# Optimization experiments

Hardware: AMD Instinct MI355X
Metric: run time of the kernel (lower is better)

The kernel has to match this reference:

```python
import jax, jax.numpy as jnp
from jax import lax
import numpy as np

B, T, Z, H, W = 4, 256, 16, 64, 64

def setup_inputs() -> dict:
    key = jax.random.key(0)
    k1, k2, k3, k4, k5 = jax.random.split(key, 5)
    # per-pixel scalar RNN parameters (nn.RNN(1, 1) per pixel)
    return {
        "x": jax.random.normal(k1, (B, T, Z, H, W), dtype=jnp.float32),
        "w_ih": jax.random.normal(k2, (Z, H, W), dtype=jnp.float32),
        "w_hh": jax.random.normal(k3, (Z, H, W), dtype=jnp.float32),
        "b_ih": jax.random.normal(k4, (Z, H, W), dtype=jnp.float32),
        "b_hh": jax.random.normal(k5, (Z, H, W), dtype=jnp.float32),
    }

def reference(x, w_ih, w_hh, b_ih, b_hh):
    # x: (B, T, Z, H, W). Per-pixel scalar tanh-RNN, h0 = 0:
    #   h_t = tanh(w_ih * x_t + b_ih + w_hh * h_{t-1} + b_hh)
    xt = jnp.moveaxis(x, 1, 0)  # (T, B, Z, H, W) for scan over time
    bias = b_ih + b_hh          # fuse biases once

    def step(h, x_t):
        h_new = jnp.tanh(x_t * w_ih + h * w_hh + bias)
        return h_new, h_new

    h0 = jnp.zeros(xt.shape[1:], dtype=x.dtype)  # (B, Z, H, W)
    _, ys = lax.scan(step, h0, xt)               # ys: (T, B, Z, H, W)
    return jnp.moveaxis(ys, 0, 1)                # (B, T, Z, H, W)
```

## Files before the change

### kernel.cpp

```cpp
#include <hip/hip_runtime.h>


#define RNN_B 4
#define RNN_T 256
#define RNN_ZHW 65536
#define RNN_PG (RNN_ZHW / 4)

__global__ __launch_bounds__(256) void pixel_rnn_kernel(
    const float* __restrict__ x,
    const float* __restrict__ w_ih,
    const float* __restrict__ w_hh,
    const float* __restrict__ b_ih,
    const float* __restrict__ b_hh,
    float* __restrict__ out)
{
    const int g  = blockIdx.x * 256 + threadIdx.x;
    const int b  = g >> 14;
    const int pg = g & (RNN_PG - 1);
    const int p  = pg << 2;

    const float4 wi = *(const float4*)(w_ih + p);
    const float4 wh = *(const float4*)(w_hh + p);
    const float4 bi = *(const float4*)(b_ih + p);
    const float4 bh = *(const float4*)(b_hh + p);
    float4 bias;
    bias.x = bi.x + bh.x;
    bias.y = bi.y + bh.y;
    bias.z = bi.z + bh.z;
    bias.w = bi.w + bh.w;

    const float4* __restrict__ xp = (const float4*)x + (size_t)b * (RNN_T * RNN_PG) + pg;
    float4* __restrict__ op       = (float4*)out     + (size_t)b * (RNN_T * RNN_PG) + pg;

    float4 h;
    h.x = 0.f; h.y = 0.f; h.z = 0.f; h.w = 0.f;

    float4 xa = xp[0];
    float4 xb = xp[RNN_PG];

    for (int t = 0; t < RNN_T; ++t) {
        const float4 xc = xa;
        xa = xb;
        int tn = t + 2;
        tn = tn < RNN_T ? tn : RNN_T - 1;
        xb = xp[(size_t)tn * RNN_PG];

        h.x = tanhf(fmaf(wi.x, xc.x, fmaf(wh.x, h.x, bias.x)));
        h.y = tanhf(fmaf(wi.y, xc.y, fmaf(wh.y, h.y, bias.y)));
        h.z = tanhf(fmaf(wi.z, xc.z, fmaf(wh.z, h.z, bias.z)));
        h.w = tanhf(fmaf(wi.w, xc.w, fmaf(wh.w, h.w, bias.w)));

        op[(size_t)t * RNN_PG] = h;
    }
}

extern "C" void kernel_launch(void* const* d_in, const int* in_sizes, int n_in,
                              void* d_out, int out_size, void* d_ws, size_t ws_size,
                              hipStream_t stream) {
    const float* x    = (const float*)d_in[0];
    const float* w_ih = (const float*)d_in[1];
    const float* w_hh = (const float*)d_in[2];
    const float* b_ih = (const float*)d_in[3];
    const float* b_hh = (const float*)d_in[4];
    float* out        = (float*)d_out;

    pixel_rnn_kernel<<<dim3(RNN_B * RNN_PG / 256), dim3(256), 0, stream>>>(
        x, w_ih, w_hh, b_ih, b_hh, out);
}
```

Before: 507.7 us.

## Halve per-thread width, deepen prefetch, use fast tanh and nontemporal memory ops

Each thread now handles two pixels instead of four, which doubles the number of threads for this otherwise very low-occupancy recurrence. The x stream is prefetched eight timesteps ahead in a register ring buffer, using nontemporal loads and stores to hide latency and avoid polluting the cache. tanhf is replaced by an exp2/reciprocal approximation to shorten the serial per-step dependency chain, at some cost in accuracy.

```diff
diff --git a/kernel.cpp b/kernel.cpp
--- a/kernel.cpp
+++ b/kernel.cpp
@@ -1,10 +1,19 @@
 #include <hip/hip_runtime.h>
 
 
-#define RNN_B 4
-#define RNN_T 256
+#define RNN_B   4
+#define RNN_T   256
 #define RNN_ZHW 65536
-#define RNN_PG (RNN_ZHW / 4)
+#define RNN_PG2 (RNN_ZHW / 2)
+#define PF_D    8
+
+typedef float f32x2 __attribute__((ext_vector_type(2)));
+
+__device__ __forceinline__ float fast_tanh(float x) {
+    float e = __builtin_amdgcn_exp2f(x * 2.885390081777927f);
+    float r = __builtin_amdgcn_rcpf(e + 1.0f);
+    return fmaf(-2.0f, r, 1.0f);
+}
 
 __global__ __launch_bounds__(256) void pixel_rnn_kernel(
     const float* __restrict__ x,
@@ -15,42 +24,41 @@
     float* __restrict__ out)
 {
     const int g  = blockIdx.x * 256 + threadIdx.x;
-    const int b  = g >> 14;
-    const int pg = g & (RNN_PG - 1);
-    const int p  = pg << 2;
+    const int b  = g >> 15;
+    const int pg = g & (RNN_PG2 - 1);
+    const int p  = pg << 1;
 
-    const float4 wi = *(const float4*)(w_ih + p);
-    const float4 wh = *(const float4*)(w_hh + p);
-    const float4 bi = *(const float4*)(b_ih + p);
-    const float4 bh = *(const float4*)(b_hh + p);
-    float4 bias;
-    bias.x = bi.x + bh.x;
-    bias.y = bi.y + bh.y;
-    bias.z = bi.z + bh.z;
-    bias.w = bi.w + bh.w;
+    const f32x2 wi = *(const f32x2*)(w_ih + p);
+    const f32x2 wh = *(const f32x2*)(w_hh + p);
+    const f32x2 bi = *(const f32x2*)(b_ih + p);
+    const f32x2 bh = *(const f32x2*)(b_hh + p);
+    const float bias_x = bi.x + bh.x;
+    const float bias_y = bi.y + bh.y;
 
-    const float4* __restrict__ xp = (const float4*)x + (size_t)b * (RNN_T * RNN_PG) + pg;
-    float4* __restrict__ op       = (float4*)out     + (size_t)b * (RNN_T * RNN_PG) + pg;
+    const f32x2* __restrict__ xp = (const f32x2*)x + (size_t)b * (RNN_T * RNN_PG2) + pg;
+    f32x2* __restrict__ op       = (f32x2*)out     + (size_t)b * (RNN_T * RNN_PG2) + pg;
 
-    float4 h;
-    h.x = 0.f; h.y = 0.f; h.z = 0.f; h.w = 0.f;
+    float hx = 0.f, hy = 0.f;
 
-    float4 xa = xp[0];
-    float4 xb = xp[RNN_PG];
+    f32x2 buf[PF_D];
+#pragma unroll
+    for (int j = 0; j < PF_D; ++j)
+        buf[j] = __builtin_nontemporal_load(xp + (size_t)j * RNN_PG2);
 
-    for (int t = 0; t < RNN_T; ++t) {
-        const float4 xc = xa;
-        xa = xb;
-        int tn = t + 2;
-        tn = tn < RNN_T ? tn : RNN_T - 1;
-        xb = xp[(size_t)tn * RNN_PG];
+    for (int t = 0; t < RNN_T; t += PF_D) {
+#pragma unroll
+        for (int j = 0; j < PF_D; ++j) {
+            const f32x2 xc = buf[j];
+            int tn = t + j + PF_D;
+            tn = tn < RNN_T ? tn : RNN_T - 1;
+            buf[j] = __builtin_nontemporal_load(xp + (size_t)tn * RNN_PG2);
 
-        h.x = tanhf(fmaf(wi.x, xc.x, fmaf(wh.x, h.x, bias.x)));
-        h.y = tanhf(fmaf(wi.y, xc.y, fmaf(wh.y, h.y, bias.y)));
-        h.z = tanhf(fmaf(wi.z, xc.z, fmaf(wh.z, h.z, bias.z)));
-        h.w = tanhf(fmaf(wi.w, xc.w, fmaf(wh.w, h.w, bias.w)));
+            hx = fast_tanh(fmaf(wi.x, xc.x, fmaf(wh.x, hx, bias_x)));
+            hy = fast_tanh(fmaf(wi.y, xc.y, fmaf(wh.y, hy, bias_y)));
 
-        op[(size_t)t * RNN_PG] = h;
+            f32x2 h2; h2.x = hx; h2.y = hy;
+            __builtin_nontemporal_store(h2, op + (size_t)(t + j) * RNN_PG2);
+        }
     }
 }
 
@@ -64,6 +72,6 @@
     const float* b_hh = (const float*)d_in[4];
     float* out        = (float*)d_out;
 
-    pixel_rnn_kernel<<<dim3(RNN_B * RNN_PG / 256), dim3(256), 0, stream>>>(
+    pixel_rnn_kernel<<<dim3(RNN_B * RNN_PG2 / 256), dim3(256), 0, stream>>>(
         x, w_ih, w_hh, b_ih, b_hh, out);
 }
```

Result: faster. 427.2 us (-15.9%).
